# Optimization experiments

Measured on AMD Instinct MI355X. Metric: run time of the kernel, lower is better.

The kernel has to match this reference:

```python
import jax, jax.numpy as jnp
import numpy as np

D_X, D_H, D_OUT = 512, 512, 512
B, T = 64, 1024


def setup_inputs() -> dict:
    key = jax.random.key(0)
    ks = jax.random.split(key, 6)
    s_x = 1.0 / np.sqrt(D_X)
    s_h = 1.0 / np.sqrt(D_H)
    return {
        "x": jax.random.normal(ks[0], (B, T, D_X), dtype=jnp.float32),
        "W_xh": jax.random.uniform(ks[1], (D_X, D_H), minval=-s_x, maxval=s_x, dtype=jnp.float32),
        "b_h": jax.random.uniform(ks[2], (D_H,), minval=-s_x, maxval=s_x, dtype=jnp.float32),
        "W_hh": jax.random.uniform(ks[3], (D_H, D_H), minval=-s_h, maxval=s_h, dtype=jnp.float32),
        "W_o": jax.random.uniform(ks[4], (D_H, D_OUT), minval=-s_h, maxval=s_h, dtype=jnp.float32),
        "b_o": jax.random.uniform(ks[5], (D_OUT,), minval=-s_h, maxval=s_h, dtype=jnp.float32),
    }


def reference(x, W_xh, b_h, W_hh, W_o, b_o):
    # x: [B, T, d_x] -> logits [B, T, d_out], last hidden [B, d_h]
    Bsz = x.shape[0]
    h0 = jnp.zeros((Bsz, W_hh.shape[0]), dtype=x.dtype)
    # Precompute input projection for all timesteps (one big GEMM).
    xW = jnp.einsum("btx,xh->bth", x, W_xh) + b_h  # [B, T, d_h]

    def step(h, xw_t):
        h_new = jnp.tanh(xw_t + h @ W_hh)  # [B, d_h]
        return h_new, h_new

    h_last, hs = jax.lax.scan(step, h0, jnp.swapaxes(xW, 0, 1))  # hs: [T, B, d_h]
    hs = jnp.swapaxes(hs, 0, 1)  # [B, T, d_h]
    logits = jnp.einsum("bth,ho->bto", hs, W_o) + b_o  # [B, T, d_out]
    return logits, h_last
```

## Files before the change

### kernel.cpp

```cpp
#include <hip/hip_runtime.h>

typedef _Float16 f16;
typedef __attribute__((ext_vector_type(4))) _Float16 f16x4;
typedef __attribute__((ext_vector_type(8))) _Float16 f16x8;
typedef __attribute__((ext_vector_type(4))) float f32x4;

__device__ __forceinline__ float tanh_fast(float x) {
  float e = __expf(2.0f * x);
  return 1.0f - 2.0f * __builtin_amdgcn_rcpf(e + 1.0f);
}

__device__ __forceinline__ void wg_sync_lds() {
  asm volatile("s_waitcnt lgkmcnt(0)" ::: "memory");
  __builtin_amdgcn_sched_barrier(0);
  __builtin_amdgcn_s_barrier();
  __builtin_amdgcn_sched_barrier(0);
}

#if defined(__has_builtin)
#if __has_builtin(__builtin_amdgcn_global_load_lds)
#define USE_GLL 1
#endif
#endif
#ifndef USE_GLL
#define USE_GLL 0
#endif

__device__ __forceinline__ void gll16(const void* g, void* l) {
#if USE_GLL
  __builtin_amdgcn_global_load_lds(
      (const __attribute__((address_space(1))) unsigned int*)g,
      (__attribute__((address_space(3))) unsigned int*)l, 16, 0, 0);
#endif
}

__global__ void k_cvt_f16(const float* __restrict__ in, f16* __restrict__ out, int n4) {
  int i = blockIdx.x * blockDim.x + threadIdx.x;
  int stride = gridDim.x * blockDim.x;
  for (; i < n4; i += stride) {
    float4 v = reinterpret_cast<const float4*>(in)[i];
    f16x4 o;
    o[0] = (f16)v.x; o[1] = (f16)v.y; o[2] = (f16)v.z; o[3] = (f16)v.w;
    *reinterpret_cast<f16x4*>(out + (size_t)i * 4) = o;
  }
}

__global__ __launch_bounds__(256) void k_transpose_cvt(const float* __restrict__ in,
                                                       f16* __restrict__ out) {
  __shared__ float tile[32][33];
  int bx = blockIdx.x & 15, by = blockIdx.x >> 4;
  int tx = threadIdx.x & 31, ty = threadIdx.x >> 5;
#pragma unroll
  for (int i = 0; i < 4; ++i)
    tile[ty + i * 8][tx] = in[(size_t)(by * 32 + ty + i * 8) * 512 + bx * 32 + tx];
  __syncthreads();
#pragma unroll
  for (int i = 0; i < 4; ++i)
    out[(size_t)(bx * 32 + ty + i * 8) * 512 + by * 32 + tx] = (f16)tile[tx][ty + i * 8];
}

__global__ __launch_bounds__(256) void k_packW(const float* __restrict__ Whh,
                                               f16* __restrict__ Wf) {
  int id = blockIdx.x * 256 + threadIdx.x;
  int c = id & 15, q = (id >> 4) & 3, kt = (id >> 6) & 15, cb = id >> 10;
  f16x8 blk;
#pragma unroll
  for (int e = 0; e < 8; ++e)
    blk[e] = (f16)Whh[(size_t)(kt * 32 + q * 8 + e) * 512 + cb * 16 + c];
  reinterpret_cast<f16x8*>(Wf)[id] = blk;
}

#define BM 128
#define BN 128
#define BK 32

template <int OUT>
__global__ __launch_bounds__(256, 2) void k_gemm(const f16* __restrict__ A,
                                                 const f16* __restrict__ Bt,
                                                 const float* __restrict__ bias,
                                                 void* __restrict__ Cout,
                                                 int M, int N, int K) {
  __shared__ __align__(16) f16 As[2][BM][BK];
  __shared__ __align__(16) f16 Bs[2][BN][BK];

  const int tid = threadIdx.x;
  const int w = tid >> 6;
  const int l = tid & 63;
  const int nbn = N / BN;
  const int bm0 = (int)(blockIdx.x / nbn) * BM;
  const int bn0 = (int)(blockIdx.x % nbn) * BN;
  const int wm = w >> 1, wn = w & 1;

  auto stage = [&](int buf, int kt) {
#pragma unroll
    for (int c = 0; c < 2; ++c) {
      const int row = c * 64 + w * 16 + (l >> 2);
      const int ke = kt + (l & 3) * 8;
#if USE_GLL
      gll16(A + (size_t)(bm0 + row) * K + ke, &As[buf][c * 64 + w * 16][0]);
      gll16(Bt + (size_t)(bn0 + row) * K + ke, &Bs[buf][c * 64 + w * 16][0]);
#else
      *(f16x8*)&As[buf][row][(l & 3) * 8] = *(const f16x8*)(A + (size_t)(bm0 + row) * K + ke);
      *(f16x8*)&Bs[buf][row][(l & 3) * 8] = *(const f16x8*)(Bt + (size_t)(bn0 + row) * K + ke);
#endif
    }
  };

  f32x4 acc[4][4] = {};
  const int nkt = K / BK;
  stage(0, 0);
  int cur = 0;
  for (int kt = 0; kt < nkt; ++kt) {
    __syncthreads();
    if (kt + 1 < nkt) stage(cur ^ 1, (kt + 1) * BK);
    f16x8 af[4], bfr[4];
#pragma unroll
    for (int m = 0; m < 4; ++m)
      af[m] = *(const f16x8*)&As[cur][wm * 64 + m * 16 + (l & 15)][(l >> 4) * 8];
#pragma unroll
    for (int n = 0; n < 4; ++n)
      bfr[n] = *(const f16x8*)&Bs[cur][wn * 64 + n * 16 + (l & 15)][(l >> 4) * 8];
#pragma unroll
    for (int m = 0; m < 4; ++m)
#pragma unroll
      for (int n = 0; n < 4; ++n)
        acc[m][n] = __builtin_amdgcn_mfma_f32_16x16x32_f16(af[m], bfr[n], acc[m][n], 0, 0, 0);
    cur ^= 1;
  }

  const int r0 = bm0 + wm * 64, c0 = bn0 + wn * 64;
#pragma unroll
  for (int n = 0; n < 4; ++n) {
    const int cc = c0 + n * 16 + (l & 15);
    const float bv = bias[cc];
#pragma unroll
    for (int m = 0; m < 4; ++m) {
      const int rr = r0 + m * 16 + ((l >> 4) << 2);
      if (OUT == 2) {
        const int b = rr >> 10, trow = rr & 1023;
        const int set = b >> 4, qq = (b >> 2) & 3, jj = b & 3;
        const int ww = (cc >> 4) & 7, ii = cc >> 7, c2 = cc & 15;
        const int tq = trow >> 2;
        f16* po = (f16*)Cout +
                  ((((((size_t)set * 256 + tq) * 8 + ww) * 4 + qq) * 4 + jj) * 16 + c2) * 16 + ii;
#pragma unroll
        for (int j = 0; j < 4; ++j) po[j * 4] = (f16)(acc[m][n][j] + bv);
      } else {
#pragma unroll
        for (int j = 0; j < 4; ++j)
          ((float*)Cout)[(size_t)(rr + j) * N + cc] = acc[m][n][j] + bv;
      }
    }
  }
}

#define SCAN_T 1024

__global__ __launch_bounds__(512, 2) void k_scan_lds(
    const f16* __restrict__ xwp,
    const f16* __restrict__ Wf,
    f16* __restrict__ hs,
    float* __restrict__ h_last) {
  const int tid = threadIdx.x;
  const int w = tid >> 6, l = tid & 63;
  const int q = l >> 4, c = l & 15;
  const int set = blockIdx.x;
  const int b0 = set * 16;

  __shared__ __align__(16) f16 wlds[8][16][4][16][8];
  __shared__ __align__(16) f16 h3[16][528];
  char* const h3b = (char*)&h3[0][0];
  char* const wldsb = (char*)&wlds[0][0][0][0][0];

  const f16x8* WfB = (const f16x8*)Wf;

  f16x8 wb0[16], wb1[16], wb2[16];
#pragma unroll
  for (int kt = 0; kt < 16; ++kt) {
    wb0[kt] = WfB[((w * 16 + kt) * 4 + q) * 16 + c];
    wb1[kt] = WfB[(((8 + w) * 16 + kt) * 4 + q) * 16 + c];
    wb2[kt] = WfB[(((16 + w) * 16 + kt) * 4 + q) * 16 + c];
  }

#pragma unroll
  for (int k2 = 0; k2 < 16; ++k2) {
    gll16(WfB + ((24 + w) * 16 + k2) * 64 + l, wldsb + (size_t)(w * 16 + k2) * 1024);
#if !USE_GLL
    ((f16x8*)wldsb)[(w * 16 + k2) * 64 + l] = WfB[((24 + w) * 16 + k2) * 64 + l];
#endif
  }
  {
    uint4* hz = (uint4*)h3b;
    for (int i = tid; i < 1056; i += 512) hz[i] = make_uint4(0u, 0u, 0u, 0u);
  }

  const int cbs[4] = {w, 8 + w, 16 + w, 24 + w};
  const int afbase = c * 1056 + 16 * (q ^ (c >> 2));
  const int wlbase = w * 16384 + q * 256 + c * 16;
  int woff[4];
#pragma unroll
  for (int i2 = 0; i2 < 4; ++i2)
    woff[i2] = (q * 4) * 1056 + (((cbs[i2] * 16 + c) ^ (q << 3)) << 1);

  const int cr = tid >> 5, cs = tid & 31;
  const int cpsrc0 = cr * 1056 + ((((cs * 2) ^ (cr >> 2))) << 4);
  const int cpsrc1 = cpsrc0 ^ 16;
  f16* const cpdst = hs + (size_t)(b0 + cr) * SCAN_T * 512 + cs * 16;

  const f16* xwbase =
      xwp + (((((size_t)set * 256 * 8 + w) * 4 + q) * 4 + 0) * 16 + c) * 16;

  f16x4 xv[2][4];
#pragma unroll
  for (int j = 0; j < 4; ++j)
    xv[0][j] = __builtin_nontemporal_load((const f16x4*)(xwbase + j * 256));

  __syncthreads();

  for (int tq = 0; tq < 256; ++tq) {
#pragma unroll
    for (int ts = 0; ts < 4; ++ts) {
      const int t = tq * 4 + ts;
      const int p = ts & 1;

      f16x8 cp0 = *(const f16x8*)(h3b + cpsrc0);
      f16x8 cp1 = *(const f16x8*)(h3b + cpsrc1);

      f32x4 acc[4];
#pragma unroll
      for (int i2 = 0; i2 < 4; ++i2)
#pragma unroll
        for (int j = 0; j < 4; ++j) acc[i2][j] = (float)xv[p][j][i2];

      {
        const int tqn = (ts == 3) ? ((tq < 255) ? tq + 1 : 255) : tq;
        const int tsn = (ts + 1) & 3;
        const f16* pb = xwbase + (size_t)tqn * 32768 + tsn * 4;
#pragma unroll
        for (int j = 0; j < 4; ++j)
          xv[p ^ 1][j] = __builtin_nontemporal_load((const f16x4*)(pb + j * 256));
      }

#pragma unroll
      for (int kt = 0; kt < 16; ++kt) {
        f16x8 af = *(const f16x8*)(h3b + afbase + kt * 64);
        f16x8 wl = *(const f16x8*)(wldsb + wlbase + kt * 1024);
        acc[0] = __builtin_amdgcn_mfma_f32_16x16x32_f16(af, wb0[kt], acc[0], 0, 0, 0);
        acc[1] = __builtin_amdgcn_mfma_f32_16x16x32_f16(af, wb1[kt], acc[1], 0, 0, 0);
        acc[2] = __builtin_amdgcn_mfma_f32_16x16x32_f16(af, wb2[kt], acc[2], 0, 0, 0);
        acc[3] = __builtin_amdgcn_mfma_f32_16x16x32_f16(af, wl, acc[3], 0, 0, 0);
      }
      wg_sync_lds();

      if (t > 0) {
        f16* d = cpdst + (size_t)(t - 1) * 512;
        __builtin_nontemporal_store(cp0, (f16x8*)d);
        __builtin_nontemporal_store(cp1, (f16x8*)(d + 8));
      }

#pragma unroll
      for (int i2 = 0; i2 < 4; ++i2)
#pragma unroll
        for (int j = 0; j < 4; ++j) {
          float hv = tanh_fast(acc[i2][j]);
          *(f16*)(h3b + woff[i2] + j * 1056) = (f16)hv;
        }
      wg_sync_lds();
    }
  }

  {
    f16x8 cp0 = *(const f16x8*)(h3b + cpsrc0);
    f16x8 cp1 = *(const f16x8*)(h3b + cpsrc1);
    f16* d = cpdst + (size_t)(SCAN_T - 1) * 512;
    __builtin_nontemporal_store(cp0, (f16x8*)d);
    __builtin_nontemporal_store(cp1, (f16x8*)(d + 8));
    float* hl = h_last + (size_t)(b0 + cr) * 512 + cs * 16;
    float4 o0, o1, o2, o3;
    o0.x = (float)cp0[0]; o0.y = (float)cp0[1]; o0.z = (float)cp0[2]; o0.w = (float)cp0[3];
    o1.x = (float)cp0[4]; o1.y = (float)cp0[5]; o1.z = (float)cp0[6]; o1.w = (float)cp0[7];
    o2.x = (float)cp1[0]; o2.y = (float)cp1[1]; o2.z = (float)cp1[2]; o2.w = (float)cp1[3];
    o3.x = (float)cp1[4]; o3.y = (float)cp1[5]; o3.z = (float)cp1[6]; o3.w = (float)cp1[7];
    *(float4*)(hl + 0) = o0;
    *(float4*)(hl + 4) = o1;
    *(float4*)(hl + 8) = o2;
    *(float4*)(hl + 12) = o3;
  }
}

extern "C" void kernel_launch(void* const* d_in, const int* in_sizes, int n_in,
                              void* d_out, int out_size, void* d_ws, size_t ws_size,
                              hipStream_t stream) {
  const float* x    = (const float*)d_in[0];
  const float* W_xh = (const float*)d_in[1];
  const float* b_h  = (const float*)d_in[2];
  const float* W_hh = (const float*)d_in[3];
  const float* W_o  = (const float*)d_in[4];
  const float* b_o  = (const float*)d_in[5];
  float* out = (float*)d_out;

  const size_t XWN = (size_t)64 * 1024 * 512;
  char* ws = (char*)d_ws;
  f16* xf   = (f16*)(ws);
  f16* xwp  = (f16*)(ws + XWN * 2);
  f16* WxhT = (f16*)(ws + XWN * 4);
  f16* WoT  = (f16*)(ws + XWN * 4 + 524288);
  f16* Wf   = (f16*)(ws + XWN * 4 + 1048576);

  k_cvt_f16<<<4096, 256, 0, stream>>>(x, xf, (int)(XWN / 4));
  k_transpose_cvt<<<256, 256, 0, stream>>>(W_xh, WxhT);
  k_transpose_cvt<<<256, 256, 0, stream>>>(W_o, WoT);
  k_packW<<<128, 256, 0, stream>>>(W_hh, Wf);

  k_gemm<2><<<2048, 256, 0, stream>>>(xf, WxhT, b_h, xwp, 65536, 512, 512);

  k_scan_lds<<<4, 512, 0, stream>>>(xwp, Wf, xf , out + XWN);

  k_gemm<0><<<2048, 256, 0, stream>>>(xf, WoT, b_o, out, 65536, 512, 512);
}
```

Measured before the change: 2.179 ms.

## Split recurrent scan across 16 workgroups with 4 batch rows each

The scan kernel now runs 16 workgroups, each handling 4 batch rows instead of 16, so the serial recurrence is spread over more compute units. The MFMA A-fragment is built by replicating the 4 real rows across the 16-row tile, and only q==0 lanes write hidden state back to the smaller LDS buffer. Each workgroup still performs the full 16-row MFMA work per step, so the extra rows are wasted compute. The per-step latency path may shrink slightly from less LDS traffic, and more CUs are active, though per-step latency still dominates.

```diff
diff --git a/kernel.cpp b/kernel.cpp
--- a/kernel.cpp
+++ b/kernel.cpp
@@ -164,11 +164,11 @@
   const int tid = threadIdx.x;
   const int w = tid >> 6, l = tid & 63;
   const int q = l >> 4, c = l & 15;
-  const int set = blockIdx.x;
-  const int b0 = set * 16;
+  const int wg = blockIdx.x;
+  const int b0 = wg * 4;
 
   __shared__ __align__(16) f16 wlds[8][16][4][16][8];
-  __shared__ __align__(16) f16 h3[16][528];
+  __shared__ __align__(16) f16 h3[4][528];
   char* const h3b = (char*)&h3[0][0];
   char* const wldsb = (char*)&wlds[0][0][0][0][0];
 
@@ -191,24 +191,30 @@
   }
   {
     uint4* hz = (uint4*)h3b;
-    for (int i = tid; i < 1056; i += 512) hz[i] = make_uint4(0u, 0u, 0u, 0u);
+    for (int i = tid; i < 264; i += 512) hz[i] = make_uint4(0u, 0u, 0u, 0u);
   }
 
   const int cbs[4] = {w, 8 + w, 16 + w, 24 + w};
-  const int afbase = c * 1056 + 16 * (q ^ (c >> 2));
+  const int r = c & 3;
+  const int afbase = r * 1056 + ((q ^ r) << 4);
   const int wlbase = w * 16384 + q * 256 + c * 16;
-  int woff[4];
-#pragma unroll
-  for (int i2 = 0; i2 < 4; ++i2)
-    woff[i2] = (q * 4) * 1056 + (((cbs[i2] * 16 + c) ^ (q << 3)) << 1);
-
-  const int cr = tid >> 5, cs = tid & 31;
-  const int cpsrc0 = cr * 1056 + ((((cs * 2) ^ (cr >> 2))) << 4);
-  const int cpsrc1 = cpsrc0 ^ 16;
+  int wbase[4], wqx[4];
+#pragma unroll
+  for (int i2 = 0; i2 < 4; ++i2) {
+    const int colW = cbs[i2] * 16 + c;
+    wbase[i2] = ((colW >> 5) << 6) + ((colW & 7) << 1);
+    wqx[i2] = ((colW >> 3) & 3) << 4;
+  }
+
+  const int cr = (tid >> 5) & 3, cs = tid & 31;
+  const int ckt = cs >> 1, cg0 = (cs & 1) * 2;
+  const int cpsrc0 = cr * 1056 + ckt * 64 + ((cg0 ^ cr) << 4);
+  const int cpsrc1 = cr * 1056 + ckt * 64 + (((cg0 + 1) ^ cr) << 4);
   f16* const cpdst = hs + (size_t)(b0 + cr) * SCAN_T * 512 + cs * 16;
 
+  const int qp = wg & 3, st = wg >> 2;
   const f16* xwbase =
-      xwp + (((((size_t)set * 256 * 8 + w) * 4 + q) * 4 + 0) * 16 + c) * 16;
+      xwp + (((((size_t)st * 256 * 8 + w) * 4 + qp) * 4 + 0) * 16 + c) * 16;
 
   f16x4 xv[2][4];
 #pragma unroll
@@ -223,8 +229,11 @@
       const int t = tq * 4 + ts;
       const int p = ts & 1;
 
-      f16x8 cp0 = *(const f16x8*)(h3b + cpsrc0);
-      f16x8 cp1 = *(const f16x8*)(h3b + cpsrc1);
+      f16x8 cp0, cp1;
+      if (tid < 128) {
+        cp0 = *(const f16x8*)(h3b + cpsrc0);
+        cp1 = *(const f16x8*)(h3b + cpsrc1);
+      }
 
       f32x4 acc[4];
 #pragma unroll
@@ -252,7 +261,7 @@
       }
       wg_sync_lds();
 
-      if (t > 0) {
+      if (t > 0 && tid < 128) {
         f16* d = cpdst + (size_t)(t - 1) * 512;
         __builtin_nontemporal_store(cp0, (f16x8*)d);
         __builtin_nontemporal_store(cp1, (f16x8*)(d + 8));
@@ -263,13 +272,14 @@
 #pragma unroll
         for (int j = 0; j < 4; ++j) {
           float hv = tanh_fast(acc[i2][j]);
-          *(f16*)(h3b + woff[i2] + j * 1056) = (f16)hv;
+          if (q == 0)
+            *(f16*)(h3b + j * 1056 + wbase[i2] + (wqx[i2] ^ (j << 4))) = (f16)hv;
         }
       wg_sync_lds();
     }
   }
 
-  {
+  if (tid < 128) {
     f16x8 cp0 = *(const f16x8*)(h3b + cpsrc0);
     f16x8 cp1 = *(const f16x8*)(h3b + cpsrc1);
     f16* d = cpdst + (size_t)(SCAN_T - 1) * 512;
@@ -314,7 +324,7 @@
 
   k_gemm<2><<<2048, 256, 0, stream>>>(xf, WxhT, b_h, xwp, 65536, 512, 512);
 
-  k_scan_lds<<<4, 512, 0, stream>>>(xwp, Wf, xf , out + XWN);
+  k_scan_lds<<<16, 512, 0, stream>>>(xwp, Wf, xf , out + XWN);
 
   k_gemm<0><<<2048, 256, 0, stream>>>(xf, WoT, b_o, out, 65536, 512, 512);
 }
```

Result: slower. 2.474 ms (+13.5%).

## Halve scan workgroup to 4 waves, each computing 8 output column tiles

Applied to the files above, without the earlier changes.

The recurrent scan kernel drops from 8 wavefronts per workgroup to 4. Each wave now produces 8 column tiles: 6 with W_hh fragments held in registers and 2 read from LDS, which doubles the LDS-resident weight share. The h row padding changes to 536 to keep LDS reads conflict-free, and hidden states are now stored straight from registers as scattered f16 stores instead of a separate LDS copy-out. Fewer waves make the per-step barriers cheaper, but each wave carries more serial MFMA work and more register pressure, and the global stores are less coalesced.

```diff
diff --git a/kernel.cpp b/kernel.cpp
--- a/kernel.cpp
+++ b/kernel.cpp
@@ -156,7 +156,7 @@
 
 #define SCAN_T 1024
 
-__global__ __launch_bounds__(512, 2) void k_scan_lds(
+__global__ __launch_bounds__(256, 1) void k_scan_w4(
     const f16* __restrict__ xwp,
     const f16* __restrict__ Wf,
     f16* __restrict__ hs,
@@ -167,53 +167,54 @@
   const int set = blockIdx.x;
   const int b0 = set * 16;
 
-  __shared__ __align__(16) f16 wlds[8][16][4][16][8];
-  __shared__ __align__(16) f16 h3[16][528];
-  char* const h3b = (char*)&h3[0][0];
-  char* const wldsb = (char*)&wlds[0][0][0][0][0];
+  __shared__ __align__(16) f16 wlds[8 * 16 * 4 * 16 * 8];
+  __shared__ __align__(16) f16 h3[16 * 536];
+  char* const h3b = (char*)h3;
+  char* const wldsb = (char*)wlds;
 
   const f16x8* WfB = (const f16x8*)Wf;
 
-  f16x8 wb0[16], wb1[16], wb2[16];
-#pragma unroll
-  for (int kt = 0; kt < 16; ++kt) {
-    wb0[kt] = WfB[((w * 16 + kt) * 4 + q) * 16 + c];
-    wb1[kt] = WfB[(((8 + w) * 16 + kt) * 4 + q) * 16 + c];
-    wb2[kt] = WfB[(((16 + w) * 16 + kt) * 4 + q) * 16 + c];
-  }
-
-#pragma unroll
-  for (int k2 = 0; k2 < 16; ++k2) {
-    gll16(WfB + ((24 + w) * 16 + k2) * 64 + l, wldsb + (size_t)(w * 16 + k2) * 1024);
+  f16x8 wr[6][16];
+#pragma unroll
+  for (int i2 = 0; i2 < 6; ++i2)
+#pragma unroll
+    for (int kt = 0; kt < 16; ++kt)
+      wr[i2][kt] = WfB[(((w + 4 * i2) * 16 + kt) * 4 + q) * 16 + c];
+
+#pragma unroll
+  for (int k2 = 0; k2 < 32; ++k2) {
+    gll16(WfB + 24 * 1024 + (w * 32 + k2) * 64 + l, wldsb + (size_t)(w * 32 + k2) * 1024);
 #if !USE_GLL
-    ((f16x8*)wldsb)[(w * 16 + k2) * 64 + l] = WfB[((24 + w) * 16 + k2) * 64 + l];
+    ((f16x8*)wldsb)[(w * 32 + k2) * 64 + l] = WfB[24 * 1024 + (w * 32 + k2) * 64 + l];
 #endif
   }
   {
     uint4* hz = (uint4*)h3b;
-    for (int i = tid; i < 1056; i += 512) hz[i] = make_uint4(0u, 0u, 0u, 0u);
-  }
-
-  const int cbs[4] = {w, 8 + w, 16 + w, 24 + w};
-  const int afbase = c * 1056 + 16 * (q ^ (c >> 2));
-  const int wlbase = w * 16384 + q * 256 + c * 16;
-  int woff[4];
-#pragma unroll
-  for (int i2 = 0; i2 < 4; ++i2)
-    woff[i2] = (q * 4) * 1056 + (((cbs[i2] * 16 + c) ^ (q << 3)) << 1);
-
-  const int cr = tid >> 5, cs = tid & 31;
-  const int cpsrc0 = cr * 1056 + ((((cs * 2) ^ (cr >> 2))) << 4);
-  const int cpsrc1 = cpsrc0 ^ 16;
-  f16* const cpdst = hs + (size_t)(b0 + cr) * SCAN_T * 512 + cs * 16;
+    for (int i = tid; i < 1072; i += 256) hz[i] = make_uint4(0u, 0u, 0u, 0u);
+  }
+
+  const int afbase = c * 1072 + ((q ^ (c >> 2)) << 4);
+  const int wlb0 = w * 16384 + q * 256 + c * 16;
+  const int wlb1 = (4 + w) * 16384 + q * 256 + c * 16;
+  int woff8[8];
+#pragma unroll
+  for (int i2 = 0; i2 < 8; ++i2)
+    woff8[i2] = q * 4 * 1072 + ((((w + 4 * i2) * 16 + c) ^ (q << 3)) << 1);
+
+  f16* hsb[4];
+#pragma unroll
+  for (int j = 0; j < 4; ++j)
+    hsb[j] = hs + (size_t)(b0 + q * 4 + j) * SCAN_T * 512 + w * 16 + c;
 
   const f16* xwbase =
-      xwp + (((((size_t)set * 256 * 8 + w) * 4 + q) * 4 + 0) * 16 + c) * 16;
-
-  f16x4 xv[2][4];
-#pragma unroll
-  for (int j = 0; j < 4; ++j)
-    xv[0][j] = __builtin_nontemporal_load((const f16x4*)(xwbase + j * 256));
+      xwp + ((((size_t)set * 256 * 8 + w) * 4 + q) * 4) * 256 + c * 16;
+
+  f16x4 xv[4][2];
+#pragma unroll
+  for (int j = 0; j < 4; ++j) {
+    xv[j][0] = __builtin_nontemporal_load((const f16x4*)(xwbase + j * 256));
+    xv[j][1] = __builtin_nontemporal_load((const f16x4*)(xwbase + 16384 + j * 256));
+  }
 
   __syncthreads();
 
@@ -221,70 +222,65 @@
 #pragma unroll
     for (int ts = 0; ts < 4; ++ts) {
       const int t = tq * 4 + ts;
-      const int p = ts & 1;
-
-      f16x8 cp0 = *(const f16x8*)(h3b + cpsrc0);
-      f16x8 cp1 = *(const f16x8*)(h3b + cpsrc1);
-
-      f32x4 acc[4];
-#pragma unroll
-      for (int i2 = 0; i2 < 4; ++i2)
-#pragma unroll
-        for (int j = 0; j < 4; ++j) acc[i2][j] = (float)xv[p][j][i2];
+
+      f32x4 acc[8];
+#pragma unroll
+      for (int i2 = 0; i2 < 8; ++i2)
+#pragma unroll
+        for (int j = 0; j < 4; ++j)
+          acc[i2][j] = (float)xv[j][i2 & 1][i2 >> 1];
 
       {
         const int tqn = (ts == 3) ? ((tq < 255) ? tq + 1 : 255) : tq;
         const int tsn = (ts + 1) & 3;
         const f16* pb = xwbase + (size_t)tqn * 32768 + tsn * 4;
 #pragma unroll
-        for (int j = 0; j < 4; ++j)
-          xv[p ^ 1][j] = __builtin_nontemporal_load((const f16x4*)(pb + j * 256));
+        for (int j = 0; j < 4; ++j) {
+          xv[j][0] = __builtin_nontemporal_load((const f16x4*)(pb + j * 256));
+          xv[j][1] = __builtin_nontemporal_load((const f16x4*)(pb + 16384 + j * 256));
+        }
       }
 
 #pragma unroll
       for (int kt = 0; kt < 16; ++kt) {
         f16x8 af = *(const f16x8*)(h3b + afbase + kt * 64);
-        f16x8 wl = *(const f16x8*)(wldsb + wlbase + kt * 1024);
-        acc[0] = __builtin_amdgcn_mfma_f32_16x16x32_f16(af, wb0[kt], acc[0], 0, 0, 0);
-        acc[1] = __builtin_amdgcn_mfma_f32_16x16x32_f16(af, wb1[kt], acc[1], 0, 0, 0);
-        acc[2] = __builtin_amdgcn_mfma_f32_16x16x32_f16(af, wb2[kt], acc[2], 0, 0, 0);
-        acc[3] = __builtin_amdgcn_mfma_f32_16x16x32_f16(af, wl, acc[3], 0, 0, 0);
+        f16x8 wl0 = *(const f16x8*)(wldsb + wlb0 + kt * 1024);
+        f16x8 wl1 = *(const f16x8*)(wldsb + wlb1 + kt * 1024);
+        acc[0] = __builtin_amdgcn_mfma_f32_16x16x32_f16(af, wr[0][kt], acc[0], 0, 0, 0);
+        acc[1] = __builtin_amdgcn_mfma_f32_16x16x32_f16(af, wr[1][kt], acc[1], 0, 0, 0);
+        acc[2] = __builtin_amdgcn_mfma_f32_16x16x32_f16(af, wr[2][kt], acc[2], 0, 0, 0);
+        acc[3] = __builtin_amdgcn_mfma_f32_16x16x32_f16(af, wr[3][kt], acc[3], 0, 0, 0);
+        acc[4] = __builtin_amdgcn_mfma_f32_16x16x32_f16(af, wr[4][kt], acc[4], 0, 0, 0);
+        acc[5] = __builtin_amdgcn_mfma_f32_16x16x32_f16(af, wr[5][kt], acc[5], 0, 0, 0);
+        acc[6] = __builtin_amdgcn_mfma_f32_16x16x32_f16(af, wl0, acc[6], 0, 0, 0);
+        acc[7] = __builtin_amdgcn_mfma_f32_16x16x32_f16(af, wl1, acc[7], 0, 0, 0);
       }
       wg_sync_lds();
 
-      if (t > 0) {
-        f16* d = cpdst + (size_t)(t - 1) * 512;
-        __builtin_nontemporal_store(cp0, (f16x8*)d);
-        __builtin_nontemporal_store(cp1, (f16x8*)(d + 8));
-      }
-
-#pragma unroll
-      for (int i2 = 0; i2 < 4; ++i2)
+#pragma unroll
+      for (int i2 = 0; i2 < 8; ++i2)
 #pragma unroll
         for (int j = 0; j < 4; ++j) {
           float hv = tanh_fast(acc[i2][j]);
-          *(f16*)(h3b + woff[i2] + j * 1056) = (f16)hv;
+          *(f16*)(h3b + woff8[i2] + j * 1072) = (f16)hv;
+          __builtin_nontemporal_store((f16)hv, hsb[j] + (size_t)t * 512 + i2 * 64);
         }
       wg_sync_lds();
     }
   }
 
   {
-    f16x8 cp0 = *(const f16x8*)(h3b + cpsrc0);
-    f16x8 cp1 = *(const f16x8*)(h3b + cpsrc1);
-    f16* d = cpdst + (size_t)(SCAN_T - 1) * 512;
-    __builtin_nontemporal_store(cp0, (f16x8*)d);
-    __builtin_nontemporal_store(cp1, (f16x8*)(d + 8));
-    float* hl = h_last + (size_t)(b0 + cr) * 512 + cs * 16;
-    float4 o0, o1, o2, o3;
-    o0.x = (float)cp0[0]; o0.y = (float)cp0[1]; o0.z = (float)cp0[2]; o0.w = (float)cp0[3];
-    o1.x = (float)cp0[4]; o1.y = (float)cp0[5]; o1.z = (float)cp0[6]; o1.w = (float)cp0[7];
-    o2.x = (float)cp1[0]; o2.y = (float)cp1[1]; o2.z = (float)cp1[2]; o2.w = (float)cp1[3];
-    o3.x = (float)cp1[4]; o3.y = (float)cp1[5]; o3.z = (float)cp1[6]; o3.w = (float)cp1[7];
-    *(float4*)(hl + 0) = o0;
-    *(float4*)(hl + 4) = o1;
-    *(float4*)(hl + 8) = o2;
-    *(float4*)(hl + 12) = o3;
+    const int m = tid >> 4, kt = tid & 15;
+    float* hl = h_last + (size_t)(b0 + m) * 512 + kt * 32;
+#pragma unroll
+    for (int kb = 0; kb < 4; ++kb) {
+      f16x8 v = *(const f16x8*)(h3b + m * 1072 + kt * 64 + (((kb ^ (m >> 2)) & 3) << 4));
+      float4 lo, hi;
+      lo.x = (float)v[0]; lo.y = (float)v[1]; lo.z = (float)v[2]; lo.w = (float)v[3];
+      hi.x = (float)v[4]; hi.y = (float)v[5]; hi.z = (float)v[6]; hi.w = (float)v[7];
+      *(float4*)(hl + kb * 8) = lo;
+      *(float4*)(hl + kb * 8 + 4) = hi;
+    }
   }
 }
 
@@ -314,7 +310,7 @@
 
   k_gemm<2><<<2048, 256, 0, stream>>>(xf, WxhT, b_h, xwp, 65536, 512, 512);
 
-  k_scan_lds<<<4, 512, 0, stream>>>(xwp, Wf, xf , out + XWN);
+  k_scan_w4<<<4, 256, 0, stream>>>(xwp, Wf, xf , out + XWN);
 
   k_gemm<0><<<2048, 256, 0, stream>>>(xf, WoT, b_o, out, 65536, 512, 512);
 }
```

Result: slower. 3.162 ms (+45.1%).
